# Kernel tuning notes

Hardware: AMD Instinct MI355X
Metric: run time of the kernel (lower is better)

## Reference

```python
import jax, jax.numpy as jnp
import numpy as np

N = 100000   # nodes
E = 800000   # directed edges (dst sorted)
D = 64       # input_dim
H = 64       # hidden_dim (must equal input_dim per fusion_layer shape)
L = 16       # latent_dim


def _lin(k, fan_in, fan_out):
    # torch nn.Linear-like init scale
    bound = 1.0 / np.sqrt(fan_in)
    kw, kb = jax.random.split(k)
    W = jax.random.uniform(kw, (fan_in, fan_out), jnp.float32, -bound, bound)
    b = jax.random.uniform(kb, (fan_out,), jnp.float32, -bound, bound)
    return W, b


def setup_inputs() -> dict:
    key = jax.random.key(0)
    ks = jax.random.split(key, 12)
    x = jax.random.normal(ks[0], (N, D), jnp.float32)
    edge_src = jax.random.randint(ks[1], (E,), 0, N, jnp.int32)
    edge_dst = jnp.sort(jax.random.randint(ks[2], (E,), 0, N, jnp.int32))
    eps = jax.random.normal(ks[3], (N, L), jnp.float32)
    W_agg, b_agg = _lin(ks[4], D, H)          # neighbor_aggregator
    W_fus, b_fus = _lin(ks[5], 2 * H, H)      # fusion_layer
    W1, b1 = _lin(ks[6], H, H)                # fc1 (input_dim==hidden_dim)
    W21, b21 = _lin(ks[7], H, L)              # fc21 -> mu
    W22, b22 = _lin(ks[8], H, L)              # fc22 -> logvar
    W3, b3 = _lin(ks[9], L, H)                # fc3
    W4, b4 = _lin(ks[10], H, D)               # fc4
    return {"x": x, "edge_src": edge_src, "edge_dst": edge_dst, "eps": eps,
            "W_agg": W_agg, "b_agg": b_agg, "W_fus": W_fus, "b_fus": b_fus,
            "W1": W1, "b1": b1, "W21": W21, "b21": b21,
            "W22": W22, "b22": b22, "W3": W3, "b3": b3, "W4": W4, "b4": b4}


def reference(x, edge_src, edge_dst, eps, W_agg, b_agg, W_fus, b_fus,
              W1, b1, W21, b21, W22, b22, W3, b3, W4, b4):
    n = x.shape[0]
    # aggregate_neighbors: segment-mean over variable-length neighbor lists;
    # nodes with no neighbors get zeros (sum==0, count clamped to 1).
    nsum = jax.ops.segment_sum(x[edge_src], edge_dst, num_segments=n)
    cnt = jax.ops.segment_sum(jnp.ones((edge_dst.shape[0],), x.dtype), edge_dst, num_segments=n)
    neighbor_avg = nsum / jnp.maximum(cnt, 1.0)[:, None]          # [N, D]
    neighbor_encoded = jax.nn.relu(neighbor_avg @ W_agg + b_agg)   # [N, H]
    combined = jnp.concatenate([x, neighbor_encoded], axis=1)      # [N, 2H]
    xf = jax.nn.relu(combined @ W_fus + b_fus)                     # [N, H]
    # VAE encode
    h1 = jax.nn.relu(xf @ W1 + b1)
    mu = h1 @ W21 + b21
    logvar = h1 @ W22 + b22
    # reparameterize (fixed eps for determinism)
    z = mu + eps * jnp.exp(0.5 * logvar)
    # decode
    h3 = jax.nn.relu(z @ W3 + b3)
    recon = jax.nn.sigmoid(h3 @ W4 + b4)
    return (recon, mu, logvar)
```

## Files before the change

### kernel.cpp

```cpp
#include <hip/hip_runtime.h>
#include <math.h>

#define N_NODES 100000
#define E_EDGES 800000
#define NT 16
#define NTILES (N_NODES / NT)
#define OFF_MU 6400000L
#define OFF_LV 8000000L

typedef __attribute__((ext_vector_type(8))) short short8;
typedef __attribute__((ext_vector_type(4))) float f32x4;
typedef __attribute__((ext_vector_type(4))) float float4v;

#define SW_AGG 0
#define SW_FUS 4096
#define SW_W1  12288
#define SW_W2  16384
#define SW_W3  18432
#define SW_W4  20480
#define SW_TOT 24576

#define PW_OFF (1 << 20)
#define XB_OFF (2 << 20)

#define PB_RS 3125
#define PB_W  7
#define PB_X  3125

__device__ __forceinline__ unsigned short f2bf(float f) {
    unsigned u = __float_as_uint(f);
    unsigned r = u + 0x7FFFu + ((u >> 16) & 1u);
    return (unsigned short)(r >> 16);
}

__device__ __forceinline__ int pidx(int row, int col) {
    const int c = ((col >> 3) ^ (row & 7));
    return row * 64 + c * 8 + (col & 7);
}

__device__ void stage_w(const float* __restrict__ W, int Ksrc, int NC,
                        int NKT, int NJT_local, int jt_off,
                        int rb, short* sw, int tid) {
    const int tot = NJT_local * NKT * 64;
    for (int s = tid; s < tot; s += 256) {
        int f = s >> 6, l = s & 63;
        int jtl = f / NKT, kt = f - jtl * NKT;
        int col = jtl * 16 + (l & 15);
        int k0 = kt * 32 + ((l >> 4) << 3);
        short8 hi;
        #pragma unroll
        for (int i = 0; i < 8; ++i) {
            float v = (k0 + i < Ksrc) ? W[(k0 + i) * NC + col] : 0.0f;
            hi[i] = (short)f2bf(v);
        }
        int fg = (jt_off + jtl) * NKT + kt;
        *(short8*)&sw[rb + fg * 512 + l * 8] = hi;
    }
}

__global__ __launch_bounds__(256) void prep(
    const int* __restrict__ edge_dst, int* __restrict__ row_start,
    const float* __restrict__ W_agg, const float* __restrict__ W_fus,
    const float* __restrict__ W1,  const float* __restrict__ W21,
    const float* __restrict__ W22, const float* __restrict__ W3,
    const float* __restrict__ W4, short* __restrict__ gw,
    const float* __restrict__ x, short* __restrict__ xbf)
{
    const int b = blockIdx.x;
    const int tid = threadIdx.x;
    if (b < PB_RS) {
        const int e = b * 256 + tid;
        if (e >= E_EDGES) return;
        int d = edge_dst[e];
        int dprev = (e == 0) ? -1 : edge_dst[e - 1];
        for (int n = dprev + 1; n <= d; ++n) row_start[n] = e;
        if (e == E_EDGES - 1) {
            for (int n = d + 1; n <= N_NODES; ++n) row_start[n] = E_EDGES;
        }
    } else if (b < PB_RS + PB_W) {
        switch (b - PB_RS) {
            case 0: stage_w(W_agg, 64, 64, 2, 4, 0, SW_AGG, gw, tid); break;
            case 1: stage_w(W_fus, 128, 64, 4, 4, 0, SW_FUS, gw, tid); break;
            case 2: stage_w(W1,   64, 64, 2, 4, 0, SW_W1,  gw, tid); break;
            case 3: stage_w(W21,  64, 16, 2, 1, 0, SW_W2,  gw, tid); break;
            case 4: stage_w(W22,  64, 16, 2, 1, 1, SW_W2,  gw, tid); break;
            case 5: stage_w(W3,   16, 64, 1, 4, 0, SW_W3,  gw, tid); break;
            case 6: stage_w(W4,   64, 64, 2, 4, 0, SW_W4,  gw, tid); break;
        }
    } else {
        const int i = (b - PB_RS - PB_W) * 256 + tid;
        if (i >= N_NODES * 8) return;
        const float4v a = ((const float4v*)x)[i * 2];
        const float4v c = ((const float4v*)x)[i * 2 + 1];
        short8 s;
        s[0] = (short)f2bf(a.x); s[1] = (short)f2bf(a.y);
        s[2] = (short)f2bf(a.z); s[3] = (short)f2bf(a.w);
        s[4] = (short)f2bf(c.x); s[5] = (short)f2bf(c.y);
        s[6] = (short)f2bf(c.z); s[7] = (short)f2bf(c.w);
        ((short8*)xbf)[i] = s;
    }
}

__device__ __forceinline__ void frags_from_xbf(const short* __restrict__ xbf,
                                               long base, int lane, short8* h) {
    const int row = lane & 15, ko = (lane >> 4) * 8;
    const short* r = xbf + (base + row) * 64;
    h[0] = *(const short8*)&r[ko];
    h[1] = *(const short8*)&r[32 + ko];
}

template<int NKT>
__device__ __forceinline__ void frags_from_planes(const short* phi, int lane,
                                                  short8* hi) {
    const int row = lane & 15;
    #pragma unroll
    for (int kt = 0; kt < NKT; ++kt) {
        const int c = kt * 4 + (lane >> 4);
        const int idx = row * 64 + ((c ^ (row & 7)) << 3);
        hi[kt] = *(const short8*)&phi[idx];
    }
}

template<int NKT>
__device__ __forceinline__ f32x4 gemm_one(const short8* ah,
                                          const short* __restrict__ sw, int rb,
                                          int jt, float bias, int lane) {
    f32x4 acc = { bias, bias, bias, bias };
    #pragma unroll
    for (int kt = 0; kt < NKT; ++kt) {
        const short8 bhi = *(const short8*)&sw[rb + (jt * NKT + kt) * 512 + lane * 8];
        acc = __builtin_amdgcn_mfma_f32_16x16x32_bf16(ah[kt], bhi, acc, 0, 0, 0);
    }
    return acc;
}

__device__ __forceinline__ void write_slab_plane(short* phi, f32x4 c, int jt,
                                                 int lane, bool relu) {
    const int g = lane >> 4, cj = lane & 15;
    const int col = jt * 16 + cj;
    #pragma unroll
    for (int r = 0; r < 4; ++r) {
        float f = relu ? fmaxf(c[r], 0.0f) : c[r];
        phi[pidx(g * 4 + r, col)] = (short)f2bf(f);
    }
}

__device__ __forceinline__ float tree16(const float* v) {
    float a0 = (v[0] + v[1]) + (v[2] + v[3]);
    float a1 = (v[4] + v[5]) + (v[6] + v[7]);
    float a2 = (v[8] + v[9]) + (v[10] + v[11]);
    float a3 = (v[12] + v[13]) + (v[14] + v[15]);
    return (a0 + a1) + (a2 + a3);
}
__device__ __forceinline__ float tree8(const float* v) {
    return ((v[0] + v[1]) + (v[2] + v[3])) + ((v[4] + v[5]) + (v[6] + v[7]));
}

__global__ __launch_bounds__(256, 8) void vae_top(
    const float* __restrict__ x,
    const short* __restrict__ xbf,
    const int* __restrict__ edge_src,
    const float* __restrict__ eps,
    const float* __restrict__ b_agg, const float* __restrict__ b_fus,
    const float* __restrict__ b1,  const float* __restrict__ b21,
    const float* __restrict__ b22, const float* __restrict__ b3,
    const float* __restrict__ b4,
    const short* __restrict__ gw,
    const int* __restrict__ row_start,
    float* __restrict__ out)
{
    __shared__ __align__(16) short sA[1024];
    __shared__ __align__(16) short sB[1024];

    const int tid  = threadIdx.x;
    const int lane = tid & 63;
    const int wid  = tid >> 6;
    const long base = (long)blockIdx.x * NT;
    const int cj = lane & 15, g = lane >> 4;

    const float bja = b_agg[wid * 16 + cj];
    const float bjf = b_fus[wid * 16 + cj];
    const float bj1 = b1[wid * 16 + cj];
    const float bj3 = b3[wid * 16 + cj];
    const float bj4 = b4[wid * 16 + cj];

    {
        const int rsv = row_start[(int)base + (lane < 17 ? lane : 16)];
        const int W0 = __builtin_amdgcn_readlane(rsv, wid * 4);
        int p0 = W0 + lane;      p0 = p0 < E_EDGES ? p0 : E_EDGES - 1;
        int p1 = W0 + 64 + lane; p1 = p1 < E_EDGES ? p1 : E_EDGES - 1;
        const int iv0 = edge_src[p0];
        const int iv1 = edge_src[p1];

        #pragma unroll
        for (int q = 0; q < 4; ++q) {
            const int node = wid * 4 + q;
            const int e0 = __builtin_amdgcn_readlane(rsv, node);
            const int e1 = __builtin_amdgcn_readlane(rsv, node + 1);
            const int deg = e1 - e0;
            const int te0 = e0 - W0;
            float sum;
            if (deg <= 8 && te0 + 7 < 128) {
                float v[8];
                #pragma unroll
                for (int i = 0; i < 8; ++i) {
                    const int te = te0 + i;
                    const int vsel = (te & 64) ? iv1 : iv0;
                    int ix = __builtin_amdgcn_readlane(vsel, te & 63);
                    const bool live = i < deg;
                    ix = live ? ix : 0;
                    float tv = x[(long)ix * 64 + lane];
                    v[i] = live ? tv : 0.0f;
                }
                sum = tree8(v);
            } else if (te0 + 15 < 128) {
                float v[16];
                #pragma unroll
                for (int i = 0; i < 16; ++i) {
                    const int te = te0 + i;
                    const int vsel = (te & 64) ? iv1 : iv0;
                    int ix = __builtin_amdgcn_readlane(vsel, te & 63);
                    const bool live = i < deg;
                    ix = live ? ix : 0;
                    float tv = x[(long)ix * 64 + lane];
                    v[i] = live ? tv : 0.0f;
                }
                sum = tree16(v);
                for (int e = e0 + 16; e < e1; ++e)
                    sum += x[(long)edge_src[e] * 64 + lane];
            } else {
                float v[16];
                #pragma unroll
                for (int i = 0; i < 16; ++i) {
                    const int ee = e0 + i;
                    const bool live = ee < e1;
                    const int ec = ee < E_EDGES ? ee : E_EDGES - 1;
                    int ix = edge_src[ec];
                    ix = live ? ix : 0;
                    float tv = x[(long)ix * 64 + lane];
                    v[i] = live ? tv : 0.0f;
                }
                sum = tree16(v);
                for (int e = e0 + 16; e < e1; ++e)
                    sum += x[(long)edge_src[e] * 64 + lane];
            }
            const float avg = sum / fmaxf((float)deg, 1.0f);
            sA[pidx(node, lane)] = (short)f2bf(avg);
        }
    }
    __syncthreads();

    short8 ah[4];
    f32x4 c;

    frags_from_planes<2>(sA, lane, ah);
    c = gemm_one<2>(ah, gw, SW_AGG, wid, bja, lane);
    write_slab_plane(sB, c, wid, lane, true);
    __syncthreads();

    frags_from_xbf(xbf, base, lane, ah);
    frags_from_planes<2>(sB, lane, ah + 2);
    c = gemm_one<4>(ah, gw, SW_FUS, wid, bjf, lane);
    write_slab_plane(sA, c, wid, lane, true);
    __syncthreads();

    frags_from_planes<2>(sA, lane, ah);
    c = gemm_one<2>(ah, gw, SW_W1, wid, bj1, lane);
    write_slab_plane(sB, c, wid, lane, true);
    __syncthreads();

    if (wid == 0) {
        frags_from_planes<2>(sB, lane, ah);
        const f32x4 cmu = gemm_one<2>(ah, gw, SW_W2, 0, b21[cj], lane);
        const f32x4 clv = gemm_one<2>(ah, gw, SW_W2, 1, b22[cj], lane);
        #pragma unroll
        for (int r = 0; r < 4; ++r) {
            const long node = base + g * 4 + r;
            out[OFF_MU + node * 16 + cj] = cmu[r];
            out[OFF_LV + node * 16 + cj] = clv[r];
            const float z = cmu[r] + eps[node * 16 + cj] * __expf(0.5f * clv[r]);
            sA[pidx(g * 4 + r, cj)] = (short)f2bf(z);
        }
    }
    __syncthreads();

    {
        short8 zh = {0,0,0,0,0,0,0,0};
        if (lane < 32) {
            const int row = lane & 15;
            const int cch = (lane >> 4);
            zh = *(const short8*)&sA[row * 64 + ((cch ^ (row & 7)) << 3)];
        }
        c = gemm_one<1>(&zh, gw, SW_W3, wid, bj3, lane);
    }
    write_slab_plane(sB, c, wid, lane, true);
    __syncthreads();

    frags_from_planes<2>(sB, lane, ah);
    c = gemm_one<2>(ah, gw, SW_W4, wid, bj4, lane);
    #pragma unroll
    for (int r = 0; r < 4; ++r) {
        const float s = 1.0f / (1.0f + __expf(-c[r]));
        out[(base + g * 4 + r) * 64 + wid * 16 + cj] = s;
    }
}

extern "C" void kernel_launch(void* const* d_in, const int* in_sizes, int n_in,
                              void* d_out, int out_size, void* d_ws, size_t ws_size,
                              hipStream_t stream) {
    const float* x        = (const float*)d_in[0];
    const int*   edge_src = (const int*)  d_in[1];
    const int*   edge_dst = (const int*)  d_in[2];
    const float* eps      = (const float*)d_in[3];
    const float* W_agg    = (const float*)d_in[4];
    const float* b_agg    = (const float*)d_in[5];
    const float* W_fus    = (const float*)d_in[6];
    const float* b_fus    = (const float*)d_in[7];
    const float* W1       = (const float*)d_in[8];
    const float* b1       = (const float*)d_in[9];
    const float* W21      = (const float*)d_in[10];
    const float* b21      = (const float*)d_in[11];
    const float* W22      = (const float*)d_in[12];
    const float* b22      = (const float*)d_in[13];
    const float* W3       = (const float*)d_in[14];
    const float* b3       = (const float*)d_in[15];
    const float* W4       = (const float*)d_in[16];
    const float* b4       = (const float*)d_in[17];
    float* out = (float*)d_out;

    int*   row_start = (int*)d_ws;
    short* gw        = (short*)((char*)d_ws + PW_OFF);
    short* xbf       = (short*)((char*)d_ws + XB_OFF);

    prep<<<PB_RS + PB_W + PB_X, 256, 0, stream>>>(edge_dst, row_start,
                                                  W_agg, W_fus, W1, W21, W22, W3, W4,
                                                  gw, x, xbf);
    vae_top<<<NTILES, 256, 0, stream>>>(x, xbf, edge_src, eps,
                                        b_agg, b_fus, b1, b21, b22, b3, b4,
                                        gw, row_start, out);
}
```

Before: 63.02 us.

## Batch neighbor gathers across four nodes and preload all weight fragments

The gather phase now handles all four nodes of a wavefront together. It loads a third block of edge indices so nearly all tiles take the fast register path, and it issues the first eight neighbor loads for every node before reducing them. This gives more memory loads in flight. All MFMA weight fragments are also loaded into registers before the barrier, so their latency overlaps the gather instead of sitting in each GEMM stage. Launch bounds drop from 8 to 6 waves to make room for the extra registers, at some cost in occupancy.

```diff
diff --git a/kernel.cpp b/kernel.cpp
--- a/kernel.cpp
+++ b/kernel.cpp
@@ -121,16 +121,18 @@
     }
 }
 
+__device__ __forceinline__ short8 ldfrag(const short* __restrict__ gw, int rb,
+                                         int fg, int lane) {
+    return *(const short8*)&gw[rb + fg * 512 + lane * 8];
+}
+
 template<int NKT>
-__device__ __forceinline__ f32x4 gemm_one(const short8* ah,
-                                          const short* __restrict__ sw, int rb,
-                                          int jt, float bias, int lane) {
+__device__ __forceinline__ f32x4 gemm_pre(const short8* ah, const short8* bh,
+                                          float bias) {
     f32x4 acc = { bias, bias, bias, bias };
     #pragma unroll
-    for (int kt = 0; kt < NKT; ++kt) {
-        const short8 bhi = *(const short8*)&sw[rb + (jt * NKT + kt) * 512 + lane * 8];
-        acc = __builtin_amdgcn_mfma_f32_16x16x32_bf16(ah[kt], bhi, acc, 0, 0, 0);
-    }
+    for (int kt = 0; kt < NKT; ++kt)
+        acc = __builtin_amdgcn_mfma_f32_16x16x32_bf16(ah[kt], bh[kt], acc, 0, 0, 0);
     return acc;
 }
 
@@ -145,6 +147,9 @@
     }
 }
 
+__device__ __forceinline__ float tree8(const float* v) {
+    return ((v[0] + v[1]) + (v[2] + v[3])) + ((v[4] + v[5]) + (v[6] + v[7]));
+}
 __device__ __forceinline__ float tree16(const float* v) {
     float a0 = (v[0] + v[1]) + (v[2] + v[3]);
     float a1 = (v[4] + v[5]) + (v[6] + v[7]);
@@ -152,11 +157,8 @@
     float a3 = (v[12] + v[13]) + (v[14] + v[15]);
     return (a0 + a1) + (a2 + a3);
 }
-__device__ __forceinline__ float tree8(const float* v) {
-    return ((v[0] + v[1]) + (v[2] + v[3])) + ((v[4] + v[5]) + (v[6] + v[7]));
-}
-
-__global__ __launch_bounds__(256, 8) void vae_top(
+
+__global__ __launch_bounds__(256, 6) void vae_top(
     const float* __restrict__ x,
     const short* __restrict__ xbf,
     const int* __restrict__ edge_src,
@@ -187,92 +189,134 @@
     {
         const int rsv = row_start[(int)base + (lane < 17 ? lane : 16)];
         const int W0 = __builtin_amdgcn_readlane(rsv, wid * 4);
-        int p0 = W0 + lane;      p0 = p0 < E_EDGES ? p0 : E_EDGES - 1;
-        int p1 = W0 + 64 + lane; p1 = p1 < E_EDGES ? p1 : E_EDGES - 1;
-        const int iv0 = edge_src[p0];
-        const int iv1 = edge_src[p1];
-
+        int e0[4], e1[4];
         #pragma unroll
         for (int q = 0; q < 4; ++q) {
-            const int node = wid * 4 + q;
-            const int e0 = __builtin_amdgcn_readlane(rsv, node);
-            const int e1 = __builtin_amdgcn_readlane(rsv, node + 1);
-            const int deg = e1 - e0;
-            const int te0 = e0 - W0;
-            float sum;
-            if (deg <= 8 && te0 + 7 < 128) {
-                float v[8];
+            e0[q] = __builtin_amdgcn_readlane(rsv, wid * 4 + q);
+            e1[q] = __builtin_amdgcn_readlane(rsv, wid * 4 + q + 1);
+        }
+        int p;
+        p = W0 + lane;        p = p < E_EDGES ? p : E_EDGES - 1; const int iv0 = edge_src[p];
+        p = W0 + 64 + lane;   p = p < E_EDGES ? p : E_EDGES - 1; const int iv1 = edge_src[p];
+        p = W0 + 128 + lane;  p = p < E_EDGES ? p : E_EDGES - 1; const int iv2 = edge_src[p];
+
+        const bool fast = (e0[3] - W0 + 15) < 192;
+
+        float sum[4];
+        if (fast) {
+            float v[4][8];
+            #pragma unroll
+            for (int q = 0; q < 4; ++q) {
+                const int te0 = e0[q] - W0;
+                const int deg = e1[q] - e0[q];
                 #pragma unroll
                 for (int i = 0; i < 8; ++i) {
                     const int te = te0 + i;
-                    const int vsel = (te & 64) ? iv1 : iv0;
+                    int vsel = (te >= 128) ? iv2 : ((te >= 64) ? iv1 : iv0);
                     int ix = __builtin_amdgcn_readlane(vsel, te & 63);
                     const bool live = i < deg;
                     ix = live ? ix : 0;
                     float tv = x[(long)ix * 64 + lane];
-                    v[i] = live ? tv : 0.0f;
+                    v[q][i] = live ? tv : 0.0f;
                 }
-                sum = tree8(v);
-            } else if (te0 + 15 < 128) {
+            }
+            #pragma unroll
+            for (int q = 0; q < 4; ++q) sum[q] = tree8(v[q]);
+            float w[4][8];
+            #pragma unroll
+            for (int q = 0; q < 4; ++q) {
+                if (e1[q] - e0[q] > 8) {
+                    const int te0 = e0[q] - W0 + 8;
+                    const int deg = e1[q] - e0[q];
+                    #pragma unroll
+                    for (int i = 0; i < 8; ++i) {
+                        const int te = te0 + i;
+                        int vsel = (te >= 128) ? iv2 : ((te >= 64) ? iv1 : iv0);
+                        int ix = __builtin_amdgcn_readlane(vsel, te & 63);
+                        const bool live = (8 + i) < deg;
+                        ix = live ? ix : 0;
+                        float tv = x[(long)ix * 64 + lane];
+                        w[q][i] = live ? tv : 0.0f;
+                    }
+                }
+            }
+            #pragma unroll
+            for (int q = 0; q < 4; ++q) {
+                if (e1[q] - e0[q] > 8) {
+                    sum[q] += tree8(w[q]);
+                    for (int e = e0[q] + 16; e < e1[q]; ++e)
+                        sum[q] += x[(long)edge_src[e] * 64 + lane];
+                }
+            }
+        } else {
+            #pragma unroll
+            for (int q = 0; q < 4; ++q) {
                 float v[16];
                 #pragma unroll
                 for (int i = 0; i < 16; ++i) {
-                    const int te = te0 + i;
-                    const int vsel = (te & 64) ? iv1 : iv0;
-                    int ix = __builtin_amdgcn_readlane(vsel, te & 63);
-                    const bool live = i < deg;
-                    ix = live ? ix : 0;
-                    float tv = x[(long)ix * 64 + lane];
-                    v[i] = live ? tv : 0.0f;
-                }
-                sum = tree16(v);
-                for (int e = e0 + 16; e < e1; ++e)
-                    sum += x[(long)edge_src[e] * 64 + lane];
-            } else {
-                float v[16];
-                #pragma unroll
-                for (int i = 0; i < 16; ++i) {
-                    const int ee = e0 + i;
-                    const bool live = ee < e1;
+                    const int ee = e0[q] + i;
+                    const bool live = ee < e1[q];
                     const int ec = ee < E_EDGES ? ee : E_EDGES - 1;
                     int ix = edge_src[ec];
                     ix = live ? ix : 0;
                     float tv = x[(long)ix * 64 + lane];
                     v[i] = live ? tv : 0.0f;
                 }
-                sum = tree16(v);
-                for (int e = e0 + 16; e < e1; ++e)
-                    sum += x[(long)edge_src[e] * 64 + lane];
+                sum[q] = tree16(v);
+                for (int e = e0[q] + 16; e < e1[q]; ++e)
+                    sum[q] += x[(long)edge_src[e] * 64 + lane];
             }
-            const float avg = sum / fmaxf((float)deg, 1.0f);
-            sA[pidx(node, lane)] = (short)f2bf(avg);
-        }
-    }
+        }
+        #pragma unroll
+        for (int q = 0; q < 4; ++q) {
+            const int deg = e1[q] - e0[q];
+            const float avg = sum[q] / fmaxf((float)deg, 1.0f);
+            sA[pidx(wid * 4 + q, lane)] = (short)f2bf(avg);
+        }
+    }
+
+    short8 w_agg[2], w_fus[4], w_w1[2], w_w3[1], w_w4[2];
+    #pragma unroll
+    for (int kt = 0; kt < 2; ++kt) w_agg[kt] = ldfrag(gw, SW_AGG, wid * 2 + kt, lane);
+    #pragma unroll
+    for (int kt = 0; kt < 4; ++kt) w_fus[kt] = ldfrag(gw, SW_FUS, wid * 4 + kt, lane);
+    #pragma unroll
+    for (int kt = 0; kt < 2; ++kt) w_w1[kt] = ldfrag(gw, SW_W1, wid * 2 + kt, lane);
+    w_w3[0] = ldfrag(gw, SW_W3, wid, lane);
+    #pragma unroll
+    for (int kt = 0; kt < 2; ++kt) w_w4[kt] = ldfrag(gw, SW_W4, wid * 2 + kt, lane);
+
     __syncthreads();
 
     short8 ah[4];
     f32x4 c;
 
     frags_from_planes<2>(sA, lane, ah);
-    c = gemm_one<2>(ah, gw, SW_AGG, wid, bja, lane);
+    c = gemm_pre<2>(ah, w_agg, bja);
     write_slab_plane(sB, c, wid, lane, true);
     __syncthreads();
 
     frags_from_xbf(xbf, base, lane, ah);
     frags_from_planes<2>(sB, lane, ah + 2);
-    c = gemm_one<4>(ah, gw, SW_FUS, wid, bjf, lane);
+    c = gemm_pre<4>(ah, w_fus, bjf);
     write_slab_plane(sA, c, wid, lane, true);
     __syncthreads();
 
     frags_from_planes<2>(sA, lane, ah);
-    c = gemm_one<2>(ah, gw, SW_W1, wid, bj1, lane);
+    c = gemm_pre<2>(ah, w_w1, bj1);
     write_slab_plane(sB, c, wid, lane, true);
     __syncthreads();
 
     if (wid == 0) {
+        short8 w21[2], w22[2];
+        #pragma unroll
+        for (int kt = 0; kt < 2; ++kt) {
+            w21[kt] = ldfrag(gw, SW_W2, kt, lane);
+            w22[kt] = ldfrag(gw, SW_W2, 2 + kt, lane);
+        }
         frags_from_planes<2>(sB, lane, ah);
-        const f32x4 cmu = gemm_one<2>(ah, gw, SW_W2, 0, b21[cj], lane);
-        const f32x4 clv = gemm_one<2>(ah, gw, SW_W2, 1, b22[cj], lane);
+        const f32x4 cmu = gemm_pre<2>(ah, w21, b21[cj]);
+        const f32x4 clv = gemm_pre<2>(ah, w22, b22[cj]);
         #pragma unroll
         for (int r = 0; r < 4; ++r) {
             const long node = base + g * 4 + r;
@@ -291,13 +335,13 @@
             const int cch = (lane >> 4);
             zh = *(const short8*)&sA[row * 64 + ((cch ^ (row & 7)) << 3)];
         }
-        c = gemm_one<1>(&zh, gw, SW_W3, wid, bj3, lane);
+        c = gemm_pre<1>(&zh, w_w3, bj3);
     }
     write_slab_plane(sB, c, wid, lane, true);
     __syncthreads();
 
     frags_from_planes<2>(sB, lane, ah);
-    c = gemm_one<2>(ah, gw, SW_W4, wid, bj4, lane);
+    c = gemm_pre<2>(ah, w_w4, bj4);
     #pragma unroll
     for (int r = 0; r < 4; ++r) {
         const float s = 1.0f / (1.0f + __expf(-c[r]));
```

Result: slower. 79.65 us (+26.4%).
